# Kernel optimization log

Measured on AMD Instinct MI355X. Metric: run time of the kernel, lower is better.

Reference implementation:

```python
import jax, jax.numpy as jnp
import numpy as np

V, E, H = 50000, 300, 256  # vocab, word dim, per-direction hidden (nfeat_sent=2H=512)
B, T = 256, 64
NEG = -1e9


def _lstm_scan(x, mask, w_ih, w_hh, b):
    """x: [T,B,E], mask: [T,B,1] float. Masked steps keep (h,c) unchanged.
    Gate order matches torch.nn.LSTM: i, f, g, o."""
    Bsz = x.shape[1]
    Hd = w_hh.shape[1]
    init = (jnp.zeros((Bsz, Hd), x.dtype), jnp.zeros((Bsz, Hd), x.dtype))

    def step(carry, inp):
        h, c = carry
        xt, mt = inp
        z = xt @ w_ih.T + h @ w_hh.T + b  # [B,4H]
        i, f, g, o = jnp.split(z, 4, axis=-1)
        i = jax.nn.sigmoid(i); f = jax.nn.sigmoid(f)
        g = jnp.tanh(g); o = jax.nn.sigmoid(o)
        c_new = f * c + i * g
        h_new = o * jnp.tanh(c_new)
        c = mt * c_new + (1.0 - mt) * c
        h = mt * h_new + (1.0 - mt) * h
        return (h, c), h

    _, hs = jax.lax.scan(step, init, (x, mask))
    return hs  # [T,B,H]


def setup_inputs() -> dict:
    key = jax.random.key(0)
    ks = jax.random.split(key, 9)
    token_ids = jax.random.randint(ks[0], (B, T), 0, V, dtype=jnp.int32)
    lengths = jax.random.randint(ks[1], (B,), 1, T + 1, dtype=jnp.int32)
    emb = jax.random.normal(ks[2], (V, E), jnp.float32) * 0.1
    s = 0.05
    w_ih_f = jax.random.normal(ks[3], (4 * H, E), jnp.float32) * s
    w_hh_f = jax.random.normal(ks[4], (4 * H, H), jnp.float32) * s
    b_f = jax.random.normal(ks[5], (4 * H,), jnp.float32) * s  # b_ih + b_hh fused
    w_ih_b = jax.random.normal(ks[6], (4 * H, E), jnp.float32) * s
    w_hh_b = jax.random.normal(ks[7], (4 * H, H), jnp.float32) * s
    b_b = jax.random.normal(ks[8], (4 * H,), jnp.float32) * s
    return {"token_ids": token_ids, "lengths": lengths, "emb": emb,
            "w_ih_f": w_ih_f, "w_hh_f": w_hh_f, "b_f": b_f,
            "w_ih_b": w_ih_b, "w_hh_b": w_hh_b, "b_b": b_b}


def reference(token_ids, lengths, emb, w_ih_f, w_hh_f, b_f, w_ih_b, w_hh_b, b_b):
    # Batched equivalent of the per-sentence loop: embed -> biLSTM -> max over time.
    x = emb[token_ids]                              # [B,T,E]
    x = jnp.swapaxes(x, 0, 1)                       # [T,B,E] (time-major)
    valid = (jnp.arange(T)[:, None] < lengths[None, :])  # [T,B]
    mask = valid.astype(x.dtype)[:, :, None]        # [T,B,1]

    h_fwd = _lstm_scan(x, mask, w_ih_f, w_hh_f, b_f)  # [T,B,H]
    # Backward direction: reverse time; masked (pad) steps leave state at zero,
    # so each sentence's backward pass starts exactly at its last real token.
    h_bwd = _lstm_scan(x[::-1], mask[::-1], w_ih_b, w_hh_b, b_b)[::-1]

    out = jnp.concatenate([h_fwd, h_bwd], axis=-1)  # [T,B,2H]
    out = jnp.where(valid[:, :, None], out, NEG)
    return jnp.max(out, axis=0)                     # [B, 2H] == [B, nfeat_sent]
```

## Files before the change

### kernel.cpp

```cpp
#include <hip/hip_runtime.h>
#include <hip/hip_bf16.h>
#include <math.h>

#define VV 50000
#define EE 300
#define HD 256
#define BB 256
#define TT 64
#define NEGV -1e9f

#define OFF_HF   0
#define OFF_CTR  524288
#define OFF_B2   526336
#define OFF_WHHF 528384
#define OFF_WIHF 1052672
#define WS_FULL_BYTES (1380352ULL * 4ULL)
#define FB_H 0
#define FB_C 262144

typedef __attribute__((ext_vector_type(8))) short bf16x8;
typedef __attribute__((ext_vector_type(4))) float f32x4;

__device__ __forceinline__ float sigf(float x) {
  return 1.f / (1.f + __expf(-x));
}
__device__ __forceinline__ float tanhfast(float x) {
  return 1.f - 2.f / (__expf(2.f * x) + 1.f);
}
__device__ __forceinline__ unsigned short f2bf(float f) {
  union { float f; unsigned u; } x;
  x.f = f;
  unsigned r = x.u + 0x7fffu + ((x.u >> 16) & 1u);
  return (unsigned short)(r >> 16);
}

__global__ __launch_bounds__(256) void prep_all(
    const float* __restrict__ whf, const float* __restrict__ whb,
    const float* __restrict__ wif, const float* __restrict__ wib,
    const float* __restrict__ bf, const float* __restrict__ bb,
    float* __restrict__ ws) {
  int idx = blockIdx.x * 256 + threadIdx.x;
  if (idx < 131072) ws[OFF_HF + idx] = 0.f;
  if (idx < 2048) {
    ((unsigned int*)(ws + OFF_CTR))[idx] = 0u;
    int dir = idx >> 10, jg = idx & 1023, j = jg >> 2, g = jg & 3;
    ws[OFF_B2 + idx] = (dir ? bb : bf)[g * HD + j];
  }
  if (idx < 65536) {
    int lane = idx & 63, kt = (idx >> 6) & 7, ngrp = (idx >> 9) & 63,
        dir = idx >> 15;
    int n = ngrp * 16 + (lane & 15);
    int j = n >> 2, g = n & 3;
    int k0 = kt * 32 + (lane >> 4) * 8;
    const float* W = dir ? whb : whf;
    const float* src = W + (size_t)((g << 8) + j) * HD + k0;
    union { unsigned short u[8]; uint4 q; } hp, lp;
#pragma unroll
    for (int e = 0; e < 8; ++e) {
      float v = src[e];
      unsigned short hh = f2bf(v);
      union { unsigned u; float f; } hf;
      hf.u = (unsigned)hh << 16;
      hp.u[e] = hh;
      lp.u[e] = f2bf(v - hf.f);
    }
    unsigned short* dst = (unsigned short*)(ws + OFF_WHHF) + (size_t)idx * 16;
    *(uint4*)dst = hp.q;
    *(uint4*)(dst + 8) = lp.q;
  }
  if (idx < 81920) {
    int lane = idx & 63;
    int f = idx >> 6;
    int kt = f % 10;
    int ngrp = (f / 10) & 63;
    int dir = f / 640;
    int n = ngrp * 16 + (lane & 15);
    int j = n >> 2, g = n & 3;
    int k0 = kt * 32 + (lane >> 4) * 8;
    const float* W = dir ? wib : wif;
    union { unsigned short u[8]; uint4 q; } p;
#pragma unroll
    for (int e = 0; e < 8; ++e) {
      int k = k0 + e;
      p.u[e] = (k < EE) ? f2bf(W[(size_t)((g << 8) + j) * EE + k])
                        : (unsigned short)0;
    }
    *(uint4*)((unsigned short*)(ws + OFF_WIHF) + (size_t)idx * 8) = p.q;
  }
}

__global__ __launch_bounds__(256) void init_kernel(float* __restrict__ ws,
                                                   float* __restrict__ out) {
  int idx = blockIdx.x * 256 + threadIdx.x;
  if (idx < 393216) ws[idx] = 0.f;
  if (idx < BB * 2 * HD) out[idx] = NEGV;
}

__global__ __launch_bounds__(512) void lstm_persist(
    const int* __restrict__ tok, const int* __restrict__ lens,
    const float* __restrict__ emb, float* __restrict__ ws,
    float* __restrict__ out) {
  const int bg = blockIdx.x;
  const int slice = blockIdx.y;
  const int dir = blockIdx.z;
  const int tid = threadIdx.x;
  const int lane = tid & 63;
  const int wv = tid >> 6;

  __shared__ __align__(16) unsigned short hfr[2][512][8];
  __shared__ __align__(16) unsigned short ebuf[2][5120];
  __shared__ unsigned int hx[16][36];

  bf16x8 whi[8], wlo[8], wih[10];
  const int ngrp = slice * 8 + wv;
  {
    const unsigned short* p = (const unsigned short*)(ws + OFF_WHHF) +
                              (size_t)(((dir * 64 + ngrp) * 8) * 64 + lane) * 16;
#pragma unroll
    for (int kt = 0; kt < 8; ++kt) {
      whi[kt] = *(const bf16x8*)(p + kt * 1024);
      wlo[kt] = *(const bf16x8*)(p + kt * 1024 + 8);
    }
    const unsigned short* q = (const unsigned short*)(ws + OFF_WIHF) +
                              (size_t)(((dir * 64 + ngrp) * 10) * 64 + lane) * 8;
#pragma unroll
    for (int kt = 0; kt < 10; ++kt) wih[kt] = *(const bf16x8*)(q + kt * 512);
  }

  const int rg = tid >> 5;
  const int k8 = tid & 31;
  const int stage_row = bg * 16 + rg;
  const int strow = stage_row * TT;
  const int o2 = 32 + (k8 & 7);
  const bool has2 = (k8 < 8);
  const int swz_r = (rg >> 1) & 3;
  const int slot1 = (k8 >> 2) * 64 + rg * 4 + ((k8 & 3) ^ swz_r);
  const int slot2 = (o2 >> 2) * 64 + rg * 4 + ((o2 & 3) ^ swz_r);

  const int q = lane & 3;
  const int base = lane & 12;
  const int r = (lane >> 4) * 4 + q;
  const int gate_row = bg * 16 + r;
  const int len = lens[gate_row];
  const int jloc = ngrp * 4 + (base >> 2);
  const int jl32 = wv * 4 + (base >> 2);
  const float4 bias4 =
      *(const float4*)(ws + OFF_B2 + dir * 1024 + ngrp * 16 + base);

  const int ld_r = lane & 15, ld_oct = lane >> 4;
  const int ld_slot = ld_r * 4 + (ld_oct ^ ((ld_r >> 1) & 3));

  unsigned int* ctr =
      (unsigned int*)(ws + OFF_CTR) + (size_t)(dir * 16 + bg) * 32;
  unsigned short* hfg = (unsigned short*)(ws + OFF_HF);

  float c = 0.f, omax = NEGV, h_prev = 0.f;

  {
    const int t0 = dir ? (TT - 1) : 0;
    const float* er = emb + (size_t)tok[strow + t0] * EE;
    float4 a0 = *(const float4*)(er + k8 * 8);
    float4 a1 = *(const float4*)(er + k8 * 8 + 4);
    union { unsigned short u[8]; uint4 q; } p;
    p.u[0] = f2bf(a0.x); p.u[1] = f2bf(a0.y); p.u[2] = f2bf(a0.z);
    p.u[3] = f2bf(a0.w); p.u[4] = f2bf(a1.x); p.u[5] = f2bf(a1.y);
    p.u[6] = f2bf(a1.z); p.u[7] = f2bf(a1.w);
    *(uint4*)&ebuf[0][slot1 * 8] = p.q;
    if (has2) {
      float4 b0 = make_float4(0.f, 0.f, 0.f, 0.f);
      float4 b1 = make_float4(0.f, 0.f, 0.f, 0.f);
      if (o2 <= 37) b0 = *(const float4*)(er + o2 * 8);
      if (o2 < 37) b1 = *(const float4*)(er + o2 * 8 + 4);
      union { unsigned short u[8]; uint4 q; } p2;
      p2.u[0] = f2bf(b0.x); p2.u[1] = f2bf(b0.y); p2.u[2] = f2bf(b0.z);
      p2.u[3] = f2bf(b0.w); p2.u[4] = f2bf(b1.x); p2.u[5] = f2bf(b1.y);
      p2.u[6] = f2bf(b1.z); p2.u[7] = f2bf(b1.w);
      *(uint4*)&ebuf[0][slot2 * 8] = p2.q;
    }
  }

  for (int s = 0; s < TT; ++s) {
    const int t = dir ? (TT - 1 - s) : s;
    const bool nstage = (s < TT - 1);
    const unsigned long long* hsrc = (const unsigned long long*)(
        hfg + (size_t)(((s & 1) * 2 + dir) * 16 + bg) * 8192);
    unsigned long long a0 = __hip_atomic_load(hsrc + 2 * tid + 0,
                                              __ATOMIC_RELAXED,
                                              __HIP_MEMORY_SCOPE_AGENT);
    unsigned long long a1 = __hip_atomic_load(hsrc + 2 * tid + 1,
                                              __ATOMIC_RELAXED,
                                              __HIP_MEMORY_SCOPE_AGENT);
    unsigned long long b0 = __hip_atomic_load(hsrc + 1024 + 2 * tid + 0,
                                              __ATOMIC_RELAXED,
                                              __HIP_MEMORY_SCOPE_AGENT);
    unsigned long long b1 = __hip_atomic_load(hsrc + 1024 + 2 * tid + 1,
                                              __ATOMIC_RELAXED,
                                              __HIP_MEMORY_SCOPE_AGENT);
    float4 pe0, pe1, qe0, qe1;
    if (nstage) {
      const int tn = dir ? (TT - 2 - s) : (s + 1);
      const float* er = emb + (size_t)tok[strow + tn] * EE;
      pe0 = *(const float4*)(er + k8 * 8);
      pe1 = *(const float4*)(er + k8 * 8 + 4);
      qe0 = make_float4(0.f, 0.f, 0.f, 0.f);
      qe1 = make_float4(0.f, 0.f, 0.f, 0.f);
      if (has2) {
        if (o2 <= 37) qe0 = *(const float4*)(er + o2 * 8);
        if (o2 < 37) qe1 = *(const float4*)(er + o2 * 8 + 4);
      }
    }
    {
      unsigned long long* l0 =
          (unsigned long long*)((char*)&hfr[0][0][0] + tid * 16);
      l0[0] = a0;
      l0[1] = a1;
      unsigned long long* l1 =
          (unsigned long long*)((char*)&hfr[0][0][0] + 8192 + tid * 16);
      l1[0] = b0;
      l1[1] = b1;
    }
    __syncthreads();
    f32x4 acc[4];
#pragma unroll
    for (int i = 0; i < 4; ++i) {
      acc[i][0] = 0.f; acc[i][1] = 0.f; acc[i][2] = 0.f; acc[i][3] = 0.f;
    }
    const unsigned short* eb = ebuf[s & 1];
#pragma unroll
    for (int kt = 0; kt < 10; ++kt) {
      bf16x8 ax = *(const bf16x8*)(eb + (kt * 64 + ld_slot) * 8);
      acc[kt & 3] =
          __builtin_amdgcn_mfma_f32_16x16x32_bf16(ax, wih[kt], acc[kt & 3], 0, 0, 0);
    }
#pragma unroll
    for (int kt = 0; kt < 8; ++kt) {
      bf16x8 ahi = *(const bf16x8*)&hfr[0][kt * 64 + ld_slot][0];
      bf16x8 alo = *(const bf16x8*)&hfr[1][kt * 64 + ld_slot][0];
      f32x4 a = acc[kt & 3];
      a = __builtin_amdgcn_mfma_f32_16x16x32_bf16(ahi, whi[kt], a, 0, 0, 0);
      a = __builtin_amdgcn_mfma_f32_16x16x32_bf16(alo, whi[kt], a, 0, 0, 0);
      a = __builtin_amdgcn_mfma_f32_16x16x32_bf16(ahi, wlo[kt], a, 0, 0, 0);
      acc[kt & 3] = a;
    }
    f32x4 zf = (acc[0] + acc[1]) + (acc[2] + acc[3]);
    float v0 = zf[0], v1 = zf[1], v2 = zf[2], v3 = zf[3];
    {
      float s0 = __shfl_xor(v1, 1), s1 = __shfl_xor(v0, 1);
      float s2 = __shfl_xor(v3, 1), s3 = __shfl_xor(v2, 1);
      const bool qb = (q & 1) != 0;
      float t0a = qb ? s0 : v0;
      float t1a = qb ? v1 : s1;
      float t2a = qb ? s2 : v2;
      float t3a = qb ? v3 : s3;
      float u0 = __shfl_xor(t2a, 2), u1 = __shfl_xor(t3a, 2);
      float u2 = __shfl_xor(t0a, 2), u3 = __shfl_xor(t1a, 2);
      const bool q2 = (q & 2) != 0;
      v0 = q2 ? u0 : t0a;
      v1 = q2 ? u1 : t1a;
      v2 = q2 ? t2a : u2;
      v3 = q2 ? t3a : u3;
    }
    float h_out = h_prev;
    if (t < len) {
      float ig = sigf(v0 + bias4.x);
      float fg = sigf(v1 + bias4.y);
      float gg = tanhfast(v2 + bias4.z);
      float og = sigf(v3 + bias4.w);
      c = fg * c + ig * gg;
      float hn = og * tanhfast(c);
      h_out = hn;
      omax = fmaxf(omax, hn);
    }
    h_prev = h_out;
    if (nstage) {
      {
        unsigned short hi = f2bf(h_out);
        union { unsigned u; float f; } hf;
        hf.u = (unsigned)hi << 16;
        unsigned short lo = f2bf(h_out - hf.f);
        hx[r][jl32] = ((unsigned)hi << 16) | (unsigned)lo;
      }
      unsigned short* ebn = ebuf[(s + 1) & 1];
      {
        union { unsigned short u[8]; uint4 q; } p;
        p.u[0] = f2bf(pe0.x); p.u[1] = f2bf(pe0.y); p.u[2] = f2bf(pe0.z);
        p.u[3] = f2bf(pe0.w); p.u[4] = f2bf(pe1.x); p.u[5] = f2bf(pe1.y);
        p.u[6] = f2bf(pe1.z); p.u[7] = f2bf(pe1.w);
        *(uint4*)&ebn[slot1 * 8] = p.q;
        if (has2) {
          union { unsigned short u[8]; uint4 q; } p2;
          p2.u[0] = f2bf(qe0.x); p2.u[1] = f2bf(qe0.y); p2.u[2] = f2bf(qe0.z);
          p2.u[3] = f2bf(qe0.w); p2.u[4] = f2bf(qe1.x); p2.u[5] = f2bf(qe1.y);
          p2.u[6] = f2bf(qe1.z); p2.u[7] = f2bf(qe1.w);
          *(uint4*)&ebn[slot2 * 8] = p2.q;
        }
      }
      __syncthreads();
      if (tid < 128) {
        const int part = tid >> 6;
        const int sl = tid & 63;
        const int wr = sl >> 2;
        const int woct = (sl & 3) ^ ((wr >> 1) & 3);
        uint4 w0 = *(const uint4*)&hx[wr][woct * 8];
        uint4 w1 = *(const uint4*)&hx[wr][woct * 8 + 4];
        unsigned long long q0, q1;
        if (part == 0) {
          q0 = ((unsigned long long)(w0.x >> 16)) |
               ((unsigned long long)(w0.y >> 16) << 16) |
               ((unsigned long long)(w0.z >> 16) << 32) |
               ((unsigned long long)(w0.w >> 16) << 48);
          q1 = ((unsigned long long)(w1.x >> 16)) |
               ((unsigned long long)(w1.y >> 16) << 16) |
               ((unsigned long long)(w1.z >> 16) << 32) |
               ((unsigned long long)(w1.w >> 16) << 48);
        } else {
          q0 = ((unsigned long long)(w0.x & 0xffffu)) |
               ((unsigned long long)(w0.y & 0xffffu) << 16) |
               ((unsigned long long)(w0.z & 0xffffu) << 32) |
               ((unsigned long long)(w0.w & 0xffffu) << 48);
          q1 = ((unsigned long long)(w1.x & 0xffffu)) |
               ((unsigned long long)(w1.y & 0xffffu) << 16) |
               ((unsigned long long)(w1.z & 0xffffu) << 32) |
               ((unsigned long long)(w1.w & 0xffffu) << 48);
        }
        unsigned long long* hdst = (unsigned long long*)(
            hfg + (size_t)((((s + 1) & 1) * 2 + dir) * 16 + bg) * 8192 +
            part * 4096 + (slice * 64 + sl) * 8);
        __hip_atomic_store(hdst + 0, q0, __ATOMIC_RELAXED,
                           __HIP_MEMORY_SCOPE_AGENT);
        __hip_atomic_store(hdst + 1, q1, __ATOMIC_RELAXED,
                           __HIP_MEMORY_SCOPE_AGENT);
      }
      asm volatile("s_waitcnt vmcnt(0)" ::: "memory");
      __syncthreads();
      if (tid == 0) {
        __hip_atomic_fetch_add(ctr, 1u, __ATOMIC_RELAXED,
                               __HIP_MEMORY_SCOPE_AGENT);
      }
      if (tid < 64) {
        const unsigned int target = 8u * (unsigned)(s + 1);
        while (__hip_atomic_load(ctr, __ATOMIC_RELAXED,
                                 __HIP_MEMORY_SCOPE_AGENT) < target) {
        }
      }
      __syncthreads();
      asm volatile("" ::: "memory");
    }
  }
  out[(size_t)gate_row * (2 * HD) + dir * HD + jloc] = omax;
}

__global__ __launch_bounds__(256) void step_fused(
    const int* __restrict__ tok, const int* __restrict__ lens,
    const float* __restrict__ emb,
    const float* __restrict__ wih_f, const float* __restrict__ whh_f,
    const float* __restrict__ bias_f,
    const float* __restrict__ wih_b, const float* __restrict__ whh_b,
    const float* __restrict__ bias_b,
    float* __restrict__ ws, float* __restrict__ out, int s) {
  const int tid = threadIdx.x;
  const int jt = blockIdx.x, bt = blockIdx.y, dir = blockIdx.z;
  const int j0 = jt * 32, b0g = bt * 16;
  const int t = (dir == 0) ? s : (TT - 1 - s);
  const float* Wih = dir ? wih_b : wih_f;
  const float* Whh = dir ? whh_b : whh_f;
  const float* bias = dir ? bias_b : bias_f;
  const float* hcur = ws + FB_H + (size_t)((s & 1) * 2 + dir) * BB * HD;
  float* hnxt = ws + FB_H + (size_t)(((s + 1) & 1) * 2 + dir) * BB * HD;
  float* cbuf = ws + FB_C + (size_t)dir * BB * HD;

  __shared__ float a_sm[16][64];
  __shared__ float w_sm[64][132];
  __shared__ float z_sm[16][132];

  const int cg = tid & 31, bgr = tid >> 5;
  float acc[2][4] = {{0.f, 0.f, 0.f, 0.f}, {0.f, 0.f, 0.f, 0.f}};

  for (int phase = 0; phase < 2; ++phase) {
    const float* W = phase ? Whh : Wih;
    const int K = phase ? HD : EE;
    for (int k0 = 0; k0 < K; k0 += 64) {
      const int klen = (K - k0) < 64 ? (K - k0) : 64;
      {
        int bl = tid >> 4, kk4 = tid & 15;
        if (kk4 * 4 < klen) {
          const float* src;
          if (phase == 0) {
            int tk = tok[(b0g + bl) * TT + t];
            src = emb + (size_t)tk * EE + k0 + kk4 * 4;
          } else {
            src = hcur + (size_t)(b0g + bl) * HD + k0 + kk4 * 4;
          }
          *(float4*)&a_sm[bl][kk4 * 4] = *(const float4*)src;
        }
      }
      for (int i = 0; i < 8; ++i) {
        int e = i * 256 + tid;
        int col = e >> 4, kk4 = e & 15;
        if (kk4 * 4 < klen) {
          int gcol = ((col >> 5) * HD) + j0 + (col & 31);
          float4 v = *(const float4*)(W + (size_t)gcol * K + k0 + kk4 * 4);
          w_sm[kk4 * 4 + 0][col] = v.x;
          w_sm[kk4 * 4 + 1][col] = v.y;
          w_sm[kk4 * 4 + 2][col] = v.z;
          w_sm[kk4 * 4 + 3][col] = v.w;
        }
      }
      __syncthreads();
      for (int k = 0; k < klen; ++k) {
        float a0 = a_sm[bgr * 2 + 0][k];
        float a1 = a_sm[bgr * 2 + 1][k];
        float4 w = *(const float4*)&w_sm[k][cg * 4];
        acc[0][0] += a0 * w.x; acc[0][1] += a0 * w.y;
        acc[0][2] += a0 * w.z; acc[0][3] += a0 * w.w;
        acc[1][0] += a1 * w.x; acc[1][1] += a1 * w.y;
        acc[1][2] += a1 * w.z; acc[1][3] += a1 * w.w;
      }
      __syncthreads();
    }
  }
  *(float4*)&z_sm[bgr * 2 + 0][cg * 4] =
      make_float4(acc[0][0], acc[0][1], acc[0][2], acc[0][3]);
  *(float4*)&z_sm[bgr * 2 + 1][cg * 4] =
      make_float4(acc[1][0], acc[1][1], acc[1][2], acc[1][3]);
  __syncthreads();
  for (int pi = 0; pi < 2; ++pi) {
    int p = pi * 256 + tid;
    int bl = p >> 5, jl = p & 31;
    int bglob = b0g + bl, jglob = j0 + jl;
    bool valid = t < lens[bglob];
    float h_old = hcur[(size_t)bglob * HD + jglob];
    float h_out = h_old;
    if (valid) {
      float zi = z_sm[bl][0 + jl] + bias[0 * HD + jglob];
      float zf = z_sm[bl][32 + jl] + bias[1 * HD + jglob];
      float zg = z_sm[bl][64 + jl] + bias[2 * HD + jglob];
      float zo = z_sm[bl][96 + jl] + bias[3 * HD + jglob];
      float ig = sigf(zi), fg = sigf(zf), gg = tanhf(zg), og = sigf(zo);
      float c_old = cbuf[(size_t)bglob * HD + jglob];
      float c_new = fg * c_old + ig * gg;
      float h_new = og * tanhf(c_new);
      cbuf[(size_t)bglob * HD + jglob] = c_new;
      h_out = h_new;
      float* op = out + (size_t)bglob * (2 * HD) + dir * HD + jglob;
      *op = fmaxf(*op, h_new);
    }
    hnxt[(size_t)bglob * HD + jglob] = h_out;
  }
}

extern "C" void kernel_launch(void* const* d_in, const int* in_sizes, int n_in,
                              void* d_out, int out_size, void* d_ws,
                              size_t ws_size, hipStream_t stream) {
  const int* tok = (const int*)d_in[0];
  const int* lens = (const int*)d_in[1];
  const float* emb = (const float*)d_in[2];
  const float* wih_f = (const float*)d_in[3];
  const float* whh_f = (const float*)d_in[4];
  const float* b_f = (const float*)d_in[5];
  const float* wih_b = (const float*)d_in[6];
  const float* whh_b = (const float*)d_in[7];
  const float* b_b = (const float*)d_in[8];
  float* out = (float*)d_out;
  float* ws = (float*)d_ws;

  const bool full = ws_size >= WS_FULL_BYTES;
  if (full) {
    hipLaunchKernelGGL(prep_all, dim3(512), dim3(256), 0, stream, whh_f,
                       whh_b, wih_f, wih_b, b_f, b_b, ws);
    hipLaunchKernelGGL(lstm_persist, dim3(16, 8, 2), dim3(512), 0, stream,
                       tok, lens, emb, ws, out);
  } else {
    hipLaunchKernelGGL(init_kernel, dim3(1536), dim3(256), 0, stream, ws, out);
    for (int s = 0; s < TT; ++s) {
      hipLaunchKernelGGL(step_fused, dim3(8, 16, 2), dim3(256), 0, stream, tok,
                         lens, emb, wih_f, whh_f, b_f, wih_b, whh_b, b_b, ws,
                         out, s);
    }
  }
}
```

Measured before the change: 218.7 us.

## Replace per-step counter barrier with per-slice flags and wave-level waits

The shared atomic counter barrier across the 8 blocks of a batch group is replaced by per-slice flags. Each wave waits only on the flag of the slice whose hidden-state chunk it reads, then loads that chunk. The input-projection MFMAs are issued before the LDS store of h, so the global load latency overlaps with compute. This removes one block-wide barrier and the contended fetch_add, but relies on relaxed atomics plus s_waitcnt for ordering, which could be fragile on memory visibility.

```diff
diff --git a/kernel.cpp b/kernel.cpp
--- a/kernel.cpp
+++ b/kernel.cpp
@@ -150,7 +150,7 @@
   const int ld_r = lane & 15, ld_oct = lane >> 4;
   const int ld_slot = ld_r * 4 + (ld_oct ^ ((ld_r >> 1) & 3));
 
-  unsigned int* ctr =
+  unsigned int* flg32 =
       (unsigned int*)(ws + OFF_CTR) + (size_t)(dir * 16 + bg) * 32;
   unsigned short* hfg = (unsigned short*)(ws + OFF_HF);
 
@@ -178,24 +178,11 @@
       *(uint4*)&ebuf[0][slot2 * 8] = p2.q;
     }
   }
+  __syncthreads();
 
   for (int s = 0; s < TT; ++s) {
     const int t = dir ? (TT - 1 - s) : s;
     const bool nstage = (s < TT - 1);
-    const unsigned long long* hsrc = (const unsigned long long*)(
-        hfg + (size_t)(((s & 1) * 2 + dir) * 16 + bg) * 8192);
-    unsigned long long a0 = __hip_atomic_load(hsrc + 2 * tid + 0,
-                                              __ATOMIC_RELAXED,
-                                              __HIP_MEMORY_SCOPE_AGENT);
-    unsigned long long a1 = __hip_atomic_load(hsrc + 2 * tid + 1,
-                                              __ATOMIC_RELAXED,
-                                              __HIP_MEMORY_SCOPE_AGENT);
-    unsigned long long b0 = __hip_atomic_load(hsrc + 1024 + 2 * tid + 0,
-                                              __ATOMIC_RELAXED,
-                                              __HIP_MEMORY_SCOPE_AGENT);
-    unsigned long long b1 = __hip_atomic_load(hsrc + 1024 + 2 * tid + 1,
-                                              __ATOMIC_RELAXED,
-                                              __HIP_MEMORY_SCOPE_AGENT);
     float4 pe0, pe1, qe0, qe1;
     if (nstage) {
       const int tn = dir ? (TT - 2 - s) : (s + 1);
@@ -209,17 +196,30 @@
         if (o2 < 37) qe1 = *(const float4*)(er + o2 * 8 + 4);
       }
     }
-    {
-      unsigned long long* l0 =
-          (unsigned long long*)((char*)&hfr[0][0][0] + tid * 16);
-      l0[0] = a0;
-      l0[1] = a1;
-      unsigned long long* l1 =
-          (unsigned long long*)((char*)&hfr[0][0][0] + 8192 + tid * 16);
-      l1[0] = b0;
-      l1[1] = b1;
-    }
-    __syncthreads();
+    if (s > 0) {
+      unsigned f = __hip_atomic_load(flg32 + wv, __ATOMIC_RELAXED,
+                                     __HIP_MEMORY_SCOPE_AGENT);
+      while (f < (unsigned)s) {
+        __builtin_amdgcn_s_sleep(2);
+        f = __hip_atomic_load(flg32 + wv, __ATOMIC_RELAXED,
+                              __HIP_MEMORY_SCOPE_AGENT);
+      }
+    }
+    asm volatile("" ::: "memory");
+    const unsigned long long* rsrc = (const unsigned long long*)(
+        hfg + (size_t)(((s & 1) * 2 + dir) * 16 + bg) * 8192);
+    unsigned long long a0 = __hip_atomic_load(rsrc + wv * 128 + lane * 2 + 0,
+                                              __ATOMIC_RELAXED,
+                                              __HIP_MEMORY_SCOPE_AGENT);
+    unsigned long long a1 = __hip_atomic_load(rsrc + wv * 128 + lane * 2 + 1,
+                                              __ATOMIC_RELAXED,
+                                              __HIP_MEMORY_SCOPE_AGENT);
+    unsigned long long b0 = __hip_atomic_load(
+        rsrc + 1024 + wv * 128 + lane * 2 + 0, __ATOMIC_RELAXED,
+        __HIP_MEMORY_SCOPE_AGENT);
+    unsigned long long b1 = __hip_atomic_load(
+        rsrc + 1024 + wv * 128 + lane * 2 + 1, __ATOMIC_RELAXED,
+        __HIP_MEMORY_SCOPE_AGENT);
     f32x4 acc[4];
 #pragma unroll
     for (int i = 0; i < 4; ++i) {
@@ -232,6 +232,14 @@
       acc[kt & 3] =
           __builtin_amdgcn_mfma_f32_16x16x32_bf16(ax, wih[kt], acc[kt & 3], 0, 0, 0);
     }
+    {
+      char* d0 = (char*)hfr + (wv * 64 + lane) * 16;
+      *(unsigned long long*)d0 = a0;
+      *(unsigned long long*)(d0 + 8) = a1;
+      *(unsigned long long*)(d0 + 8192) = b0;
+      *(unsigned long long*)(d0 + 8200) = b1;
+    }
+    __syncthreads();
 #pragma unroll
     for (int kt = 0; kt < 8; ++kt) {
       bf16x8 ahi = *(const bf16x8*)&hfr[0][kt * 64 + ld_slot][0];
@@ -296,55 +304,44 @@
         }
       }
       __syncthreads();
-      if (tid < 128) {
-        const int part = tid >> 6;
-        const int sl = tid & 63;
+      if (wv == 0) {
+        const int sl = lane;
         const int wr = sl >> 2;
         const int woct = (sl & 3) ^ ((wr >> 1) & 3);
         uint4 w0 = *(const uint4*)&hx[wr][woct * 8];
         uint4 w1 = *(const uint4*)&hx[wr][woct * 8 + 4];
-        unsigned long long q0, q1;
-        if (part == 0) {
-          q0 = ((unsigned long long)(w0.x >> 16)) |
-               ((unsigned long long)(w0.y >> 16) << 16) |
-               ((unsigned long long)(w0.z >> 16) << 32) |
-               ((unsigned long long)(w0.w >> 16) << 48);
-          q1 = ((unsigned long long)(w1.x >> 16)) |
-               ((unsigned long long)(w1.y >> 16) << 16) |
-               ((unsigned long long)(w1.z >> 16) << 32) |
-               ((unsigned long long)(w1.w >> 16) << 48);
-        } else {
-          q0 = ((unsigned long long)(w0.x & 0xffffu)) |
-               ((unsigned long long)(w0.y & 0xffffu) << 16) |
-               ((unsigned long long)(w0.z & 0xffffu) << 32) |
-               ((unsigned long long)(w0.w & 0xffffu) << 48);
-          q1 = ((unsigned long long)(w1.x & 0xffffu)) |
-               ((unsigned long long)(w1.y & 0xffffu) << 16) |
-               ((unsigned long long)(w1.z & 0xffffu) << 32) |
-               ((unsigned long long)(w1.w & 0xffffu) << 48);
+        unsigned long long qh0 = ((unsigned long long)(w0.x >> 16)) |
+                                 ((unsigned long long)(w0.y >> 16) << 16) |
+                                 ((unsigned long long)(w0.z >> 16) << 32) |
+                                 ((unsigned long long)(w0.w >> 16) << 48);
+        unsigned long long qh1 = ((unsigned long long)(w1.x >> 16)) |
+                                 ((unsigned long long)(w1.y >> 16) << 16) |
+                                 ((unsigned long long)(w1.z >> 16) << 32) |
+                                 ((unsigned long long)(w1.w >> 16) << 48);
+        unsigned long long ql0 = ((unsigned long long)(w0.x & 0xffffu)) |
+                                 ((unsigned long long)(w0.y & 0xffffu) << 16) |
+                                 ((unsigned long long)(w0.z & 0xffffu) << 32) |
+                                 ((unsigned long long)(w0.w & 0xffffu) << 48);
+        unsigned long long ql1 = ((unsigned long long)(w1.x & 0xffffu)) |
+                                 ((unsigned long long)(w1.y & 0xffffu) << 16) |
+                                 ((unsigned long long)(w1.z & 0xffffu) << 32) |
+                                 ((unsigned long long)(w1.w & 0xffffu) << 48);
+        unsigned long long* hdst = (unsigned long long*)(
+            hfg + (size_t)((((s + 1) & 1) * 2 + dir) * 16 + bg) * 8192);
+        __hip_atomic_store(hdst + slice * 128 + sl * 2 + 0, qh0,
+                           __ATOMIC_RELAXED, __HIP_MEMORY_SCOPE_AGENT);
+        __hip_atomic_store(hdst + slice * 128 + sl * 2 + 1, qh1,
+                           __ATOMIC_RELAXED, __HIP_MEMORY_SCOPE_AGENT);
+        __hip_atomic_store(hdst + 1024 + slice * 128 + sl * 2 + 0, ql0,
+                           __ATOMIC_RELAXED, __HIP_MEMORY_SCOPE_AGENT);
+        __hip_atomic_store(hdst + 1024 + slice * 128 + sl * 2 + 1, ql1,
+                           __ATOMIC_RELAXED, __HIP_MEMORY_SCOPE_AGENT);
+        asm volatile("s_waitcnt vmcnt(0)" ::: "memory");
+        if (tid == 0) {
+          __hip_atomic_store(flg32 + slice, (unsigned)(s + 1),
+                             __ATOMIC_RELAXED, __HIP_MEMORY_SCOPE_AGENT);
         }
-        unsigned long long* hdst = (unsigned long long*)(
-            hfg + (size_t)((((s + 1) & 1) * 2 + dir) * 16 + bg) * 8192 +
-            part * 4096 + (slice * 64 + sl) * 8);
-        __hip_atomic_store(hdst + 0, q0, __ATOMIC_RELAXED,
-                           __HIP_MEMORY_SCOPE_AGENT);
-        __hip_atomic_store(hdst + 1, q1, __ATOMIC_RELAXED,
-                           __HIP_MEMORY_SCOPE_AGENT);
-      }
-      asm volatile("s_waitcnt vmcnt(0)" ::: "memory");
-      __syncthreads();
-      if (tid == 0) {
-        __hip_atomic_fetch_add(ctr, 1u, __ATOMIC_RELAXED,
-                               __HIP_MEMORY_SCOPE_AGENT);
-      }
-      if (tid < 64) {
-        const unsigned int target = 8u * (unsigned)(s + 1);
-        while (__hip_atomic_load(ctr, __ATOMIC_RELAXED,
-                                 __HIP_MEMORY_SCOPE_AGENT) < target) {
-        }
-      }
-      __syncthreads();
-      asm volatile("" ::: "memory");
+      }
     }
   }
   out[(size_t)gate_row * (2 * HD) + dir * HD + jloc] = omax;
```

New measurement: 268.6 us. 22.8% more time.
